# Kernel tuning notes

Hardware: AMD Instinct MI355X
Metric: run time of the kernel (lower is better)

The kernel has to match this reference:

```python
import jax, jax.numpy as jnp
import numpy as np

# Dimensions: E experts, T tokens, K hidden, I intermediate (gate+up fused -> 2I)
E, T, K, I = 8, 4096, 2048, 768
TOP_K = 2


def setup_inputs() -> dict:
    key = jax.random.key(0)
    ks = jax.random.split(key, 6)
    hidden_states = jax.random.normal(ks[0], (T, K), dtype=jnp.float32)
    router_logits = jax.random.normal(ks[1], (T, E), dtype=jnp.float32)
    # 2-bit codes {0,1,2} <-> ternary {-1,0,+1} (pack_i2s_weights maps w+1)
    w13_q = jax.random.randint(ks[2], (E, 2 * I, K), 0, 3, dtype=jnp.int32)
    w2_q = jax.random.randint(ks[3], (E, K, I), 0, 3, dtype=jnp.int32)
    # per-input-column alpha scales (always positive, realistic magnitude)
    alpha13 = jax.random.uniform(ks[4], (E, K), dtype=jnp.float32) * 0.04 + 0.01
    alpha2 = jax.random.uniform(ks[5], (E, I), dtype=jnp.float32) * 0.04 + 0.01
    return {
        "hidden_states": hidden_states,
        "router_logits": router_logits,
        "w13_q": w13_q,
        "w2_q": w2_q,
        "alpha13": alpha13,
        "alpha2": alpha2,
    }


def reference(hidden_states, router_logits, w13_q, w2_q, alpha13, alpha2):
    # --- routing: softmax + top-k + renormalize ---
    probs = jax.nn.softmax(router_logits, axis=-1)              # [T, E]
    topk_w, topk_ids = jax.lax.top_k(probs, TOP_K)              # [T, k]
    topk_w = topk_w / jnp.sum(topk_w, axis=-1, keepdims=True)
    # dense combine weights [T, E]; zero for unselected experts
    gates = jnp.sum(
        jax.nn.one_hot(topk_ids, E, dtype=topk_w.dtype) * topk_w[..., None],
        axis=1,
    )

    # --- dequant ternary weights: W = (code - 1) * alpha[input_col] ---
    W13 = (w13_q.astype(jnp.float32) - 1.0) * alpha13[:, None, :]  # [E, 2I, K]
    W2 = (w2_q.astype(jnp.float32) - 1.0) * alpha2[:, None, :]     # [E, K, I]

    # --- grouped expert GEMMs (x @ W^T per expert) ---
    h = jnp.einsum("tk,enk->etn", hidden_states, W13)            # [E, T, 2I]
    g, u = jnp.split(h, 2, axis=-1)
    a = jax.nn.silu(g) * u                                       # [E, T, I]
    y = jnp.einsum("eti,eni->etn", a, W2)                        # [E, T, K]

    # --- combine with routing weights ---
    out = jnp.einsum("te,etk->tk", gates, y)                     # [T, K]
    return out
```

## Files before the change

### kernel.cpp

```cpp
#include <hip/hip_runtime.h>
#include <math.h>

#define E_ 8
#define T_ 4096
#define K_ 2048
#define I_ 768
#define TWOI 1536
#define NPAIR (2*T_)

typedef unsigned short u16;
typedef signed char i8;
typedef __attribute__((ext_vector_type(8))) __bf16 bf16x8;
typedef __attribute__((ext_vector_type(4))) float f32x4;
typedef __attribute__((ext_vector_type(4))) int i32x4;
typedef __attribute__((ext_vector_type(4))) unsigned u32x4;
typedef __attribute__((ext_vector_type(8))) u16 u16x8;
typedef __attribute__((ext_vector_type(4))) u16 u16x4;
typedef __attribute__((ext_vector_type(4))) int int4v;
typedef __attribute__((ext_vector_type(4))) float float4v;

typedef __attribute__((address_space(3))) char lds_c;
typedef __attribute__((address_space(1))) const char g_c;

__device__ inline void gld16(const void* g, void* l) {
    __builtin_amdgcn_global_load_lds((g_c*)g, (lds_c*)l, 16, 0, 0);
}

__device__ inline u16 f2bf(float x) {
    unsigned u = __builtin_bit_cast(unsigned, x);
    unsigned r = 0x7fffu + ((u >> 16) & 1u);
    u += r;
    return (u16)(u >> 16);
}
__device__ inline float bf2f(u16 b) {
    unsigned u = ((unsigned)b) << 16;
    return __builtin_bit_cast(float, u);
}
__device__ inline unsigned pack4(int4v q) {
    return (unsigned)((unsigned char)(char)(q[0] - 1))
         | ((unsigned)((unsigned char)(char)(q[1] - 1)) << 8)
         | ((unsigned)((unsigned char)(char)(q[2] - 1)) << 16)
         | ((unsigned)((unsigned char)(char)(q[3] - 1)) << 24);
}

#define CVT13_B 6144
#define CVT2_B  3072
#define QX_BASE (CVT13_B + CVT2_B)
__global__ __launch_bounds__(256) void k_fusedA(
    const int* __restrict__ w13q, const int* __restrict__ w2q,
    const float* __restrict__ alpha2, const float* __restrict__ logits,
    const float* __restrict__ x, const float* __restrict__ alpha13,
    i8* __restrict__ wc13, u16* __restrict__ wb2,
    i8* __restrict__ xq, float* __restrict__ sx,
    int* __restrict__ tid2, float* __restrict__ tw, int* __restrict__ cursors)
{
    __shared__ float wm[4];
    int bid = blockIdx.x;
    int tid = threadIdx.x;
    if (bid < CVT13_B) {
        long base = (long)bid * 4096;
        const int4v* qp = (const int4v*)(w13q + base);
#pragma unroll
        for (int p = 0; p < 4; ++p) {
            int4v q = qp[p * 256 + tid];
            *(unsigned*)(wc13 + base + p * 1024 + tid * 4) = pack4(q);
        }
    } else if (bid < QX_BASE) {
        long base = (long)(bid - CVT13_B) * 4096;
        const int4v* qp = (const int4v*)(w2q + base);
#pragma unroll
        for (int p = 0; p < 4; ++p) {
            long g = base + p * 1024 + tid * 4;
            int i = (int)(g % I_);
            int e = (int)(g / ((long)K_ * I_));
            int4v q = qp[p * 256 + tid];
            float4v a = *(const float4v*)(alpha2 + e * I_ + i);
            u16x4 r;
            r[0] = f2bf((float)(q[0] - 1) * a[0]);
            r[1] = f2bf((float)(q[1] - 1) * a[1]);
            r[2] = f2bf((float)(q[2] - 1) * a[2]);
            r[3] = f2bf((float)(q[3] - 1) * a[3]);
            *(u16x4*)(wb2 + g) = r;
        }
    } else {
        int p = bid - QX_BASE;
        int t = p >> 1, s = p & 1;
        float l[E_];
#pragma unroll
        for (int e = 0; e < E_; ++e) l[e] = logits[t * E_ + e];
        int e0 = 0; float mx0 = l[0];
#pragma unroll
        for (int e = 1; e < E_; ++e) if (l[e] > mx0) { mx0 = l[e]; e0 = e; }
        int e1 = -1; float mx1 = -1e30f;
#pragma unroll
        for (int e = 0; e < E_; ++e) if (e != e0 && l[e] > mx1) { mx1 = l[e]; e1 = e; }
        int e = s ? e1 : e0;

        float xa[2][4];
#pragma unroll
        for (int c = 0; c < 2; ++c) {
            int off = c * 1024 + tid * 4;
            float4v xv = *(const float4v*)(x + (long)t * K_ + off);
            float4v av = *(const float4v*)(alpha13 + (long)e * K_ + off);
#pragma unroll
            for (int j = 0; j < 4; ++j) xa[c][j] = xv[j] * av[j];
        }
        float m = 0.f;
#pragma unroll
        for (int c = 0; c < 2; ++c)
#pragma unroll
            for (int j = 0; j < 4; ++j) m = fmaxf(m, fabsf(xa[c][j]));
#pragma unroll
        for (int off = 32; off >= 1; off >>= 1) m = fmaxf(m, __shfl_xor(m, off));
        if ((tid & 63) == 0) wm[tid >> 6] = m;
        __syncthreads();
        m = fmaxf(fmaxf(wm[0], wm[1]), fmaxf(wm[2], wm[3]));
        float inv = (m > 0.f) ? 127.0f / m : 0.f;
#pragma unroll
        for (int c = 0; c < 2; ++c) {
            unsigned pk = 0;
#pragma unroll
            for (int j = 0; j < 4; ++j) {
                int qv = __float2int_rn(xa[c][j] * inv);
                pk |= ((unsigned)(unsigned char)(char)qv) << (8 * j);
            }
            *(unsigned*)(xq + (long)p * K_ + c * 1024 + tid * 4) = pk;
        }
        if (tid == 0) {
            sx[p] = m / 127.0f;
            if (!s) {
                tid2[2 * t + 0] = e0; tid2[2 * t + 1] = e1;
                float w0 = 1.0f / (1.0f + expf(mx1 - mx0));
                tw[2 * t + 0] = w0; tw[2 * t + 1] = 1.0f - w0;
            }
        }
        if (p == 0 && tid < E_) cursors[tid] = 0;
    }
}

__global__ __launch_bounds__(256) void k_lists2(
    const int* __restrict__ tid2, int* __restrict__ offsets,
    int* __restrict__ cursors, int* __restrict__ pairTok)
{
    int tid = threadIdx.x;
    int c[E_];
#pragma unroll
    for (int e = 0; e < E_; ++e) c[e] = 0;
    for (int j = 0; j < 32; ++j) {
        int v = tid2[tid * 32 + j];
#pragma unroll
        for (int e = 0; e < E_; ++e) c[e] += (v == e) ? 1 : 0;
    }
#pragma unroll
    for (int e = 0; e < E_; ++e)
#pragma unroll
        for (int off = 32; off >= 1; off >>= 1)
            c[e] += __shfl_xor(c[e], off);
    __shared__ int ws[4][E_];
    __shared__ int offs[E_ + 1];
    if ((tid & 63) == 0)
#pragma unroll
        for (int e = 0; e < E_; ++e) ws[tid >> 6][e] = c[e];
    __syncthreads();
    if (tid == 0) {
        int s2 = 0;
        for (int e = 0; e < E_; ++e) {
            int ce = ws[0][e] + ws[1][e] + ws[2][e] + ws[3][e];
            offs[e] = s2; s2 += ce;
        }
        offs[E_] = s2;
        if (blockIdx.x == 0)
            for (int e = 0; e <= E_; ++e) offsets[e] = offs[e];
    }
    __syncthreads();
    int t = blockIdx.x * 256 + tid;
#pragma unroll
    for (int s = 0; s < 2; ++s) {
        int e = tid2[t * 2 + s];
        int pos = atomicAdd(&cursors[e], 1);
        pairTok[offs[e] + pos] = (t << 1) | s;
    }
}

__global__ __launch_bounds__(512, 2) void k_g1i8(
    const i8* __restrict__ A,
    const i8* __restrict__ B,
    const int* __restrict__ pairTok, const int* __restrict__ offsets,
    const float* __restrict__ sx,
    u16* __restrict__ C)
{
    int bid = blockIdx.x;
    int e  = bid & 7;
    int r_ = bid >> 3;
    int mc = r_ / 6;
    int nch = r_ % 6;
    int base = offsets[e];
    int cnt  = offsets[e + 1] - base;
    int m0 = mc * 256;
    if (m0 >= cnt) return;
    int n0 = nch * 128;

    __shared__ __attribute__((aligned(16))) i8 SHM[131072];
    i8* As = SHM;
    i8* Bs = SHM + 65536;

    int tid = threadIdx.x;
    int lane = tid & 63;
    int wid = tid >> 6;
    int wr = wid >> 2, wc = wid & 3;
    int l15 = lane & 15;

    const i8* srcA[4];
    const i8* srcB[4];
#pragma unroll
    for (int j = 0; j < 4; ++j) {
        int chunk = j * 512 + tid;
        int row = chunk >> 3, ch = chunk & 7;
        int colsw = (ch ^ (row & 7)) * 16;
        int ra = m0 + row; if (ra >= cnt) ra = cnt - 1;
        srcA[j] = A + (long)pairTok[base + ra] * K_ + colsw;
        int grow = e * TWOI + (row >> 7) * I_ + n0 + (row & 127);
        srcB[j] = B + (long)grow * K_ + colsw;
    }

    auto stage = [&](int bs, int t) {
        int k0 = t * 128;
        i8* dA = As + bs * 32768;
        i8* dB = Bs + bs * 32768;
#pragma unroll
        for (int j = 0; j < 4; ++j) {
            gld16(srcA[j] + k0, dA + j * 8192 + tid * 16);
            gld16(srcB[j] + k0, dB + j * 8192 + tid * 16);
        }
    };

    int kq16 = ((lane >> 4) & 3) * 16;

    i32x4 a[4][2], b[4][2];
    i32x4 acc[8][4];
#pragma unroll
    for (int mf = 0; mf < 8; ++mf)
#pragma unroll
        for (int nf = 0; nf < 4; ++nf)
            acc[mf][nf] = (i32x4){0, 0, 0, 0};

    auto rdA = [&](int bs, int h64) {
#pragma unroll
        for (int mf = 0; mf < 4; ++mf) {
            int row = wr * 128 + h64 + mf * 16 + l15;
            const i8* p = As + bs * 32768 + row * 128;
            int xr = (row & 7) << 4;
            a[mf][0] = *(const i32x4*)(p + ((kq16) ^ xr));
            a[mf][1] = *(const i32x4*)(p + ((64 + kq16) ^ xr));
        }
    };
    auto rdB = [&](int bs) {
#pragma unroll
        for (int nf = 0; nf < 4; ++nf) {
            int row = wc * 64 + nf * 16 + l15;
            const i8* p = Bs + bs * 32768 + row * 128;
            int xr = (row & 7) << 4;
            b[nf][0] = *(const i32x4*)(p + ((kq16) ^ xr));
            b[nf][1] = *(const i32x4*)(p + ((64 + kq16) ^ xr));
        }
    };
    auto mm = [&](int mh) {
#pragma unroll
        for (int ks = 0; ks < 2; ++ks)
#pragma unroll
            for (int mf = 0; mf < 4; ++mf)
#pragma unroll
                for (int nf = 0; nf < 4; ++nf)
                    acc[mh * 4 + mf][nf] = __builtin_amdgcn_mfma_i32_16x16x64_i8(
                        a[mf][ks], b[nf][ks], acc[mh * 4 + mf][nf], 0, 0, 0);
    };
    auto compute = [&](int bs) {
        rdB(bs);
        rdA(bs, 0);
        mm(0);
        rdA(bs, 64);
        mm(1);
    };

    stage(0, 0);
    __syncthreads();
#pragma unroll 1
    for (int t = 0; t < 16; t += 2) {
        stage(1, t + 1);
        compute(0);
        __syncthreads();
        if (t + 2 < 16) stage(0, t + 2);
        compute(1);
        __syncthreads();
    }

    u16* flat = (u16*)SHM;
#pragma unroll
    for (int mf = 0; mf < 8; ++mf)
#pragma unroll
        for (int nf = 0; nf < 4; ++nf)
#pragma unroll
            for (int rg = 0; rg < 4; ++rg) {
                int row = wr * 128 + mf * 16 + (lane >> 4) * 4 + rg;
                int col = wc * 64 + nf * 16 + l15;
                flat[row * 256 + (col ^ ((row & 7) << 3))] = f2bf((float)acc[mf][nf][rg]);
            }
    __syncthreads();
    int row = tid >> 1;
    if (m0 + row < cnt) {
        float s = sx[pairTok[base + m0 + row]];
        int xr = (row & 7) << 3;
        int half = tid & 1;
        u16* dst = C + (long)(base + m0 + row) * I_ + n0 + half * 64;
#pragma unroll
        for (int jj = 0; jj < 8; ++jj) {
            u16x8 gv = *(const u16x8*)&flat[row * 256 + ((half * 64 + jj * 8) ^ xr)];
            u16x8 uv = *(const u16x8*)&flat[row * 256 + ((128 + half * 64 + jj * 8) ^ xr)];
            u16x8 r;
#pragma unroll
            for (int q = 0; q < 8; ++q) {
                float g = bf2f(gv[q]) * s, u = bf2f(uv[q]) * s;
                r[q] = f2bf(g / (1.0f + expf(-g)) * u);
            }
            *(u16x8*)(dst + jj * 8) = r;
        }
    }
}

__global__ __launch_bounds__(512, 2) void k_g2(
    const u16* __restrict__ A,
    const u16* __restrict__ B,
    const int* __restrict__ pairTok, const int* __restrict__ offsets,
    u16* __restrict__ C)
{
    int bid = blockIdx.x;
    int e  = bid & 7;
    int r_ = bid >> 3;
    int mc = r_ >> 3;
    int nch = r_ & 7;
    int base = offsets[e];
    int cnt  = offsets[e + 1] - base;
    int m0 = mc * 256;
    if (m0 >= cnt) return;
    int n0 = nch * 256;

    __shared__ __attribute__((aligned(16))) char SHM[131072];
    u16* ldsA = (u16*)SHM;
    u16* ldsB = (u16*)(SHM + 65536);

    int tid = threadIdx.x;
    int lane = tid & 63;
    int wid = tid >> 6;
    int wr = wid >> 2, wc = wid & 3;
    int l15 = lane & 15;

    const u16* srcA[2][2];
    const u16* srcB[2][2];
#pragma unroll
    for (int h = 0; h < 2; ++h)
#pragma unroll
        for (int j = 0; j < 2; ++j) {
            int slot = j * 512 + tid;
            int row = slot >> 3, ch = slot & 7;
            int colsw = (ch ^ (row & 7)) * 8;
            int ra = m0 + h * 128 + row;
            if (ra >= cnt) ra = cnt - 1;
            srcA[h][j] = A + (long)(base + ra) * I_ + colsw;
            long brow = (long)e * K_ + n0 + h * 128 + row;
            srcB[h][j] = B + brow * (long)I_ + colsw;
        }
    int d0 = tid * 8, d1 = (512 + tid) * 8;

    auto stage = [&](int bs, int t) {
        int k0 = t * 64;
        u16* dA = ldsA + bs * 16384;
        u16* dB = ldsB + bs * 16384;
#pragma unroll
        for (int h = 0; h < 2; ++h) {
            gld16(srcA[h][0] + k0, dA + h * 8192 + d0);
            gld16(srcA[h][1] + k0, dA + h * 8192 + d1);
            gld16(srcB[h][0] + k0, dB + h * 8192 + d0);
            gld16(srcB[h][1] + k0, dB + h * 8192 + d1);
        }
    };

    int kc0 = ((((lane >> 4) & 3) * 8)) ^ ((lane & 7) * 8);
    int kc1 = (32 + (((lane >> 4) & 3) * 8)) ^ ((lane & 7) * 8);

    bf16x8 a[4][2], b[4][2];
    f32x4 acc[8][4];
#pragma unroll
    for (int mf = 0; mf < 8; ++mf)
#pragma unroll
        for (int nf = 0; nf < 4; ++nf)
            acc[mf][nf] = (f32x4){0.f, 0.f, 0.f, 0.f};

    auto rdA = [&](int bs, int h64) {
#pragma unroll
        for (int mf = 0; mf < 4; ++mf) {
            const u16* p = ldsA + bs * 16384 + (wr * 128 + h64 + mf * 16 + l15) * 64;
            a[mf][0] = __builtin_bit_cast(bf16x8, *(const u16x8*)(p + kc0));
            a[mf][1] = __builtin_bit_cast(bf16x8, *(const u16x8*)(p + kc1));
        }
    };
    auto rdB = [&](int bs) {
#pragma unroll
        for (int nf = 0; nf < 4; ++nf) {
            const u16* p = ldsB + bs * 16384 + (wc * 64 + nf * 16 + l15) * 64;
            b[nf][0] = __builtin_bit_cast(bf16x8, *(const u16x8*)(p + kc0));
            b[nf][1] = __builtin_bit_cast(bf16x8, *(const u16x8*)(p + kc1));
        }
    };
    auto mm = [&](int mh) {
#pragma unroll
        for (int ks = 0; ks < 2; ++ks)
#pragma unroll
            for (int mf = 0; mf < 4; ++mf)
#pragma unroll
                for (int nf = 0; nf < 4; ++nf)
                    acc[mh * 4 + mf][nf] = __builtin_amdgcn_mfma_f32_16x16x32_bf16(
                        a[mf][ks], b[nf][ks], acc[mh * 4 + mf][nf], 0, 0, 0);
    };
    auto compute = [&](int bs) {
        rdB(bs);
        rdA(bs, 0);
        mm(0);
        rdA(bs, 64);
        mm(1);
    };

    stage(0, 0);
    __syncthreads();
#pragma unroll 1
    for (int t = 0; t < 12; t += 2) {
        stage(1, t + 1);
        compute(0);
        __syncthreads();
        if (t + 2 < 12) stage(0, t + 2);
        compute(1);
        __syncthreads();
    }

    u16* flat = (u16*)SHM;
#pragma unroll
    for (int mf = 0; mf < 8; ++mf)
#pragma unroll
        for (int nf = 0; nf < 4; ++nf)
#pragma unroll
            for (int rg = 0; rg < 4; ++rg) {
                int row = wr * 128 + mf * 16 + (lane >> 4) * 4 + rg;
                int col = wc * 64 + nf * 16 + l15;
                flat[row * 256 + (col ^ ((row & 7) << 3))] = f2bf(acc[mf][nf][rg]);
            }
    __syncthreads();
    int row = tid >> 1;
    if (m0 + row < cnt) {
        int xr = (row & 7) << 3;
        int half = tid & 1;
        int pt = pairTok[base + m0 + row];
        u16* dst = C + (long)pt * K_ + n0 + half * 128;
#pragma unroll
        for (int jj = 0; jj < 16; ++jj) {
            *(u16x8*)(dst + jj * 8) =
                *(const u16x8*)&flat[row * 256 + ((half * 128 + jj * 8) ^ xr)];
        }
    }
}

__global__ void k_combine(const u16* __restrict__ yb, const float* __restrict__ tw,
                          float* __restrict__ out) {
    long idx = ((long)blockIdx.x * 256 + threadIdx.x) * 8;
    int t = (int)(idx >> 11);
    float w0 = tw[t * 2 + 0];
    float w1 = tw[t * 2 + 1];
    u16x8 y0 = *(const u16x8*)(yb + (long)(2 * t) * K_ + (idx & (K_ - 1)));
    u16x8 y1 = *(const u16x8*)(yb + (long)(2 * t + 1) * K_ + (idx & (K_ - 1)));
    float4v o0, o1;
#pragma unroll
    for (int j = 0; j < 4; ++j) o0[j] = w0 * bf2f(y0[j]) + w1 * bf2f(y1[j]);
#pragma unroll
    for (int j = 0; j < 4; ++j) o1[j] = w0 * bf2f(y0[4 + j]) + w1 * bf2f(y1[4 + j]);
    *(float4v*)(out + idx) = o0;
    *(float4v*)(out + idx + 4) = o1;
}

extern "C" void kernel_launch(void* const* d_in, const int* in_sizes, int n_in,
                              void* d_out, int out_size, void* d_ws, size_t ws_size,
                              hipStream_t stream) {
    const float* x       = (const float*)d_in[0];
    const float* logits  = (const float*)d_in[1];
    const int*   w13q    = (const int*)d_in[2];
    const int*   w2q     = (const int*)d_in[3];
    const float* alpha13 = (const float*)d_in[4];
    const float* alpha2  = (const float*)d_in[5];
    float* out = (float*)d_out;

    char* ws = (char*)d_ws;
    i8*  wc13 = (i8*)(ws);
    u16* wb2  = (u16*)(ws + 50331648);
    i8*  xq   = (i8*)(ws + 75497472);
    u16* ab   = (u16*)(ws + 92274688);
    u16* yb   = (u16*)(ws + 104857600);
    int* pairTok = (int*)(ws + 138412032);
    int* tid2    = pairTok + NPAIR;
    float* tw    = (float*)(tid2 + NPAIR);
    int* counts  = (int*)(tw + NPAIR);
    int* offsets = counts + 8;
    int* cursors = offsets + 9;
    float* sx    = (float*)(cursors + 8);

    k_fusedA<<<QX_BASE + NPAIR, 256, 0, stream>>>(
        w13q, w2q, alpha2, logits, x, alpha13, wc13, wb2, xq, sx, tid2, tw, cursors);

    k_lists2<<<T_ / 256, 256, 0, stream>>>(tid2, offsets, cursors, pairTok);

    k_g1i8<<<8 * (T_ / 256) * 6, 512, 0, stream>>>(xq, wc13, pairTok, offsets, sx, ab);

    k_g2<<<8 * (T_ / 256) * (K_ / 256), 512, 0, stream>>>(ab, wb2, pairTok, offsets, yb);

    k_combine<<<((long)T_ * K_) / 8 / 256, 256, 0, stream>>>(yb, tw, out);
}
```

Before: 192.9 us.

## Restructure prep kernel into grid-stride loops with one wave per token

The prep kernel now launches a fixed 2048 blocks, each running grid-stride loops over the w13 and w2 weight conversions with nontemporal loads. Token quantization is remapped from one 256-thread block per (token, expert) pair to one 64-lane wave per token. That wave reuses the loaded activation row for both selected experts and reduces with shuffles only, with no shared-memory barrier. The aim is to cut block-launch overhead and redundant reads of the activations, at the cost of fewer threads in flight per token and longer serial loops per thread.

Measured after the change: 191.7 us. No clear change (-0.6%).

```diff
diff --git a/kernel.cpp b/kernel.cpp
--- a/kernel.cpp
+++ b/kernel.cpp
@@ -43,9 +43,7 @@
          | ((unsigned)((unsigned char)(char)(q[3] - 1)) << 24);
 }
 
-#define CVT13_B 6144
-#define CVT2_B  3072
-#define QX_BASE (CVT13_B + CVT2_B)
+#define NBLK 2048
 __global__ __launch_bounds__(256) void k_fusedA(
     const int* __restrict__ w13q, const int* __restrict__ w2q,
     const float* __restrict__ alpha2, const float* __restrict__ logits,
@@ -54,26 +52,31 @@
     i8* __restrict__ xq, float* __restrict__ sx,
     int* __restrict__ tid2, float* __restrict__ tw, int* __restrict__ cursors)
 {
-    __shared__ float wm[4];
+    int tid = threadIdx.x;
     int bid = blockIdx.x;
-    int tid = threadIdx.x;
-    if (bid < CVT13_B) {
-        long base = (long)bid * 4096;
-        const int4v* qp = (const int4v*)(w13q + base);
-#pragma unroll
-        for (int p = 0; p < 4; ++p) {
-            int4v q = qp[p * 256 + tid];
-            *(unsigned*)(wc13 + base + p * 1024 + tid * 4) = pack4(q);
-        }
-    } else if (bid < QX_BASE) {
-        long base = (long)(bid - CVT13_B) * 4096;
-        const int4v* qp = (const int4v*)(w2q + base);
-#pragma unroll
-        for (int p = 0; p < 4; ++p) {
-            long g = base + p * 1024 + tid * 4;
+    if (bid == 0 && tid < E_) cursors[tid] = 0;
+
+    {
+        const int4v* src = (const int4v*)w13q;
+        unsigned* dst = (unsigned*)wc13;
+        const long n = 6291456;
+        const long stride = (long)NBLK * 256;
+#pragma unroll 2
+        for (long u = (long)bid * 256 + tid; u < n; u += stride) {
+            int4v q = __builtin_nontemporal_load(src + u);
+            dst[u] = pack4(q);
+        }
+    }
+    {
+        const int4v* src = (const int4v*)w2q;
+        const long n = 3145728;
+        const long stride = (long)NBLK * 256;
+#pragma unroll 2
+        for (long u = (long)bid * 256 + tid; u < n; u += stride) {
+            long g = u * 4;
             int i = (int)(g % I_);
             int e = (int)(g / ((long)K_ * I_));
-            int4v q = qp[p * 256 + tid];
+            int4v q = __builtin_nontemporal_load(src + u);
             float4v a = *(const float4v*)(alpha2 + e * I_ + i);
             u16x4 r;
             r[0] = f2bf((float)(q[0] - 1) * a[0]);
@@ -82,59 +85,61 @@
             r[3] = f2bf((float)(q[3] - 1) * a[3]);
             *(u16x4*)(wb2 + g) = r;
         }
-    } else {
-        int p = bid - QX_BASE;
-        int t = p >> 1, s = p & 1;
-        float l[E_];
-#pragma unroll
-        for (int e = 0; e < E_; ++e) l[e] = logits[t * E_ + e];
-        int e0 = 0; float mx0 = l[0];
-#pragma unroll
-        for (int e = 1; e < E_; ++e) if (l[e] > mx0) { mx0 = l[e]; e0 = e; }
-        int e1 = -1; float mx1 = -1e30f;
-#pragma unroll
-        for (int e = 0; e < E_; ++e) if (e != e0 && l[e] > mx1) { mx1 = l[e]; e1 = e; }
-        int e = s ? e1 : e0;
-
-        float xa[2][4];
-#pragma unroll
-        for (int c = 0; c < 2; ++c) {
-            int off = c * 1024 + tid * 4;
-            float4v xv = *(const float4v*)(x + (long)t * K_ + off);
-            float4v av = *(const float4v*)(alpha13 + (long)e * K_ + off);
-#pragma unroll
-            for (int j = 0; j < 4; ++j) xa[c][j] = xv[j] * av[j];
-        }
-        float m = 0.f;
-#pragma unroll
-        for (int c = 0; c < 2; ++c)
-#pragma unroll
-            for (int j = 0; j < 4; ++j) m = fmaxf(m, fabsf(xa[c][j]));
-#pragma unroll
-        for (int off = 32; off >= 1; off >>= 1) m = fmaxf(m, __shfl_xor(m, off));
-        if ((tid & 63) == 0) wm[tid >> 6] = m;
-        __syncthreads();
-        m = fmaxf(fmaxf(wm[0], wm[1]), fmaxf(wm[2], wm[3]));
-        float inv = (m > 0.f) ? 127.0f / m : 0.f;
-#pragma unroll
-        for (int c = 0; c < 2; ++c) {
-            unsigned pk = 0;
-#pragma unroll
-            for (int j = 0; j < 4; ++j) {
-                int qv = __float2int_rn(xa[c][j] * inv);
-                pk |= ((unsigned)(unsigned char)(char)qv) << (8 * j);
+    }
+    {
+        int wv = bid * 4 + (tid >> 6);
+        if (wv < T_) {
+            int lane = tid & 63;
+            int t = wv;
+            float l[E_];
+#pragma unroll
+            for (int e = 0; e < E_; ++e) l[e] = logits[t * E_ + e];
+            int e0 = 0; float mx0 = l[0];
+#pragma unroll
+            for (int e = 1; e < E_; ++e) if (l[e] > mx0) { mx0 = l[e]; e0 = e; }
+            int e1 = -1; float mx1 = -1e30f;
+#pragma unroll
+            for (int e = 0; e < E_; ++e) if (e != e0 && l[e] > mx1) { mx1 = l[e]; e1 = e; }
+
+            float4v xr[8];
+#pragma unroll
+            for (int c = 0; c < 8; ++c)
+                xr[c] = *(const float4v*)(x + (long)t * K_ + c * 256 + lane * 4);
+
+#pragma unroll
+            for (int s = 0; s < 2; ++s) {
+                int e = s ? e1 : e0;
+                int p = 2 * t + s;
+                float4v xa[8];
+                float m = 0.f;
+#pragma unroll
+                for (int c = 0; c < 8; ++c) {
+                    float4v a = *(const float4v*)(alpha13 + (long)e * K_ + c * 256 + lane * 4);
+                    xa[c] = xr[c] * a;
+#pragma unroll
+                    for (int j = 0; j < 4; ++j) m = fmaxf(m, fabsf(xa[c][j]));
+                }
+#pragma unroll
+                for (int off = 32; off >= 1; off >>= 1) m = fmaxf(m, __shfl_xor(m, off));
+                float inv = (m > 0.f) ? 127.0f / m : 0.f;
+#pragma unroll
+                for (int c = 0; c < 8; ++c) {
+                    unsigned pk = 0;
+#pragma unroll
+                    for (int j = 0; j < 4; ++j) {
+                        int qv = __float2int_rn(xa[c][j] * inv);
+                        pk |= ((unsigned)(unsigned char)(char)qv) << (8 * j);
+                    }
+                    *(unsigned*)(xq + (long)p * K_ + c * 256 + lane * 4) = pk;
+                }
+                if (lane == 0) sx[p] = m / 127.0f;
             }
-            *(unsigned*)(xq + (long)p * K_ + c * 1024 + tid * 4) = pk;
-        }
-        if (tid == 0) {
-            sx[p] = m / 127.0f;
-            if (!s) {
+            if (lane == 0) {
                 tid2[2 * t + 0] = e0; tid2[2 * t + 1] = e1;
                 float w0 = 1.0f / (1.0f + expf(mx1 - mx0));
                 tw[2 * t + 0] = w0; tw[2 * t + 1] = 1.0f - w0;
             }
         }
-        if (p == 0 && tid < E_) cursors[tid] = 0;
     }
 }
 
@@ -509,7 +514,7 @@
     int* cursors = offsets + 9;
     float* sx    = (float*)(cursors + 8);
 
-    k_fusedA<<<QX_BASE + NPAIR, 256, 0, stream>>>(
+    k_fusedA<<<NBLK, 256, 0, stream>>>(
         w13q, w2q, alpha2, logits, x, alpha13, wc13, wb2, xq, sx, tid2, tw, cursors);
 
     k_lists2<<<T_ / 256, 256, 0, stream>>>(tid2, offsets, cursors, pairTok);
```
